# Performance work log

Hardware: AMD Instinct MI355X
Metric: run time of the kernel (lower is better)

Reference implementation:

```python
import jax, jax.numpy as jnp
import numpy as np

N, E = 20000, 320000
IN, HID, OUT, H = 128, 32, 1, 4
EPS = 1e-16  # PyG softmax epsilon


def _p(key, shape, scale=0.05):
    return jax.random.normal(key, shape, dtype=jnp.float32) * scale


def setup_inputs() -> dict:
    key = jax.random.key(0)
    ks = jax.random.split(key, 20)
    d = {
        "x": jax.random.normal(ks[0], (N, IN), dtype=jnp.float32),
        "edge_src": jax.random.randint(ks[1], (E,), 0, N, dtype=jnp.int32),
        "edge_dst": jax.random.randint(ks[2], (E,), 0, N, dtype=jnp.int32),
        # layer 1: TransformerConv(IN, HID, H)  ->  [N, H*HID]
        "W1q": _p(ks[3], (IN, H * HID)), "b1q": jnp.zeros((H * HID,), jnp.float32),
        "W1k": _p(ks[4], (IN, H * HID)), "b1k": jnp.zeros((H * HID,), jnp.float32),
        "W1v": _p(ks[5], (IN, H * HID)), "b1v": jnp.zeros((H * HID,), jnp.float32),
        "W1s": _p(ks[6], (IN, H * HID)), "b1s": jnp.zeros((H * HID,), jnp.float32),
        # layer 2: TransformerConv(H*HID, OUT, H) -> [N, H*OUT]
        "W2q": _p(ks[7], (H * HID, H * OUT)), "b2q": jnp.zeros((H * OUT,), jnp.float32),
        "W2k": _p(ks[8], (H * HID, H * OUT)), "b2k": jnp.zeros((H * OUT,), jnp.float32),
        "W2v": _p(ks[9], (H * HID, H * OUT)), "b2v": jnp.zeros((H * OUT,), jnp.float32),
        "W2s": _p(ks[10], (H * HID, H * OUT)), "b2s": jnp.zeros((H * OUT,), jnp.float32),
        # final nn.Linear(heads, 1)
        "Wl": _p(ks[11], (H, 1)), "bl": jnp.zeros((1,), jnp.float32),
    }
    return d


def transformer_conv(x, src, dst, Wq, bq, Wk, bk, Wv, bv, Ws, bs, heads, ch):
    n = x.shape[0]
    q = (x @ Wq + bq).reshape(n, heads, ch)
    k = (x @ Wk + bk).reshape(n, heads, ch)
    v = (x @ Wv + bv).reshape(n, heads, ch)
    qi, kj, vj = q[dst], k[src], v[src]            # [E,H,C] gathers
    score = (qi * kj).sum(-1) / jnp.sqrt(jnp.float32(ch))  # [E,H]
    m = jax.ops.segment_max(score, dst, num_segments=n)    # segment softmax by target
    e = jnp.exp(score - m[dst])
    s = jax.ops.segment_sum(e, dst, num_segments=n)
    alpha = e / (s[dst] + EPS)                              # [E,H]
    agg = jax.ops.segment_sum(alpha[:, :, None] * vj, dst, num_segments=n)  # [N,H,C]
    return agg.reshape(n, heads * ch) + x @ Ws + bs          # concat + root skip


def reference(x, edge_src, edge_dst,
              W1q, b1q, W1k, b1k, W1v, b1v, W1s, b1s,
              W2q, b2q, W2k, b2k, W2v, b2v, W2s, b2s,
              Wl, bl):
    h = transformer_conv(x, edge_src, edge_dst, W1q, b1q, W1k, b1k, W1v, b1v, W1s, b1s, H, HID)
    h = jax.nn.relu(h)  # dropout is identity in eval
    h = transformer_conv(h, edge_src, edge_dst, W2q, b2q, W2k, b2k, W2v, b2v, W2s, b2s, H, OUT)
    y = h @ Wl + bl                      # [N,1]
    return y.mean(axis=0, keepdims=True)  # [1,1]
```

## Files before the change

### kernel.cpp

```cpp
#include <hip/hip_runtime.h>
#include <math.h>

static constexpr float EPS_PYG = 1e-16f;
static constexpr float INV_SQRT32 = 0.17677669529663687f;

__global__ void deg_kernel(const int* __restrict__ dst, int* __restrict__ deg, int E) {
    int e = blockIdx.x * blockDim.x + threadIdx.x;
    if (e < E) atomicAdd(&deg[dst[e]], 1);
}

__global__ __launch_bounds__(1024) void scan_kernel(const int* __restrict__ deg,
                                                    int* __restrict__ row_off, int n) {
    const int t = threadIdx.x;
    const int CH = (n + 1023) >> 10;
    const int base = t * CH;
    int vals[32];
    int sum = 0;
#pragma unroll 4
    for (int i = 0; i < CH; ++i) {
        int idx = base + i;
        int v = (idx < n) ? deg[idx] : 0;
        sum += v;
        vals[i] = sum;
    }
    const int lane = t & 63;
    const int wid = t >> 6;
    int wsum = sum;
#pragma unroll
    for (int off = 1; off < 64; off <<= 1) {
        int o = __shfl_up(wsum, off, 64);
        if (lane >= off) wsum += o;
    }
    __shared__ int wtot[16];
    if (lane == 63) wtot[wid] = wsum;
    __syncthreads();
    if (t < 64) {
        int v = (t < 16) ? wtot[t] : 0;
        int inc = v;
#pragma unroll
        for (int off = 1; off < 16; off <<= 1) {
            int o = __shfl_up(inc, off, 64);
            if (t >= off) inc += o;
        }
        if (t < 16) wtot[t] = inc - v;
    }
    __syncthreads();
    const int toff = wtot[wid] + (wsum - sum);
    if (t == 0) row_off[0] = 0;
#pragma unroll 4
    for (int i = 0; i < CH; ++i) {
        int idx = base + i;
        if (idx < n) row_off[idx + 1] = toff + vals[i];
    }
}

__global__ void scatter_kernel(const int* __restrict__ src, const int* __restrict__ dst,
                               const int* __restrict__ row_off, int* __restrict__ cursor,
                               int* __restrict__ csr_src, int E) {
    int e = blockIdx.x * blockDim.x + threadIdx.x;
    if (e < E) {
        int d = dst[e];
        int pos = row_off[d] + atomicAdd(&cursor[d], 1);
        csr_src[pos] = src[e];
    }
}

__global__ __launch_bounds__(256) void gemm1_kernel(
    const float* __restrict__ X,
    const float* __restrict__ Wq, const float* __restrict__ Wk,
    const float* __restrict__ Wv, const float* __restrict__ Wsk,
    const float* __restrict__ bq, const float* __restrict__ bk,
    const float* __restrict__ bv, const float* __restrict__ bsk,
    float* __restrict__ Q, float* __restrict__ KV, float* __restrict__ S, int n)
{
    __shared__ float Xs[64][68];
    __shared__ float Wt[64][64];

    const int mat    = blockIdx.y >> 1;
    const int colblk = blockIdx.y & 1;
    const float* W    = (mat == 0) ? Wq : (mat == 1) ? Wk : (mat == 2) ? Wv : Wsk;
    const float* bias = (mat == 0) ? bq : (mat == 1) ? bk : (mat == 2) ? bv : bsk;
    float*       C    = (mat == 0) ? Q  : (mat == 3) ? S  : KV;
    const int strideF4 = (mat == 1 || mat == 2) ? 64 : 32;
    const int baseF4   = (mat == 2) ? 32 : 0;

    const int r0  = blockIdx.x * 64;
    const int tid = threadIdx.x;
    const int i0 = (tid >> 4) * 4;
    const int j0 = (tid & 15) * 4;
    float acc[4][4] = {};

#pragma unroll
    for (int kb = 0; kb < 2; ++kb) {
        for (int f = tid; f < 1024; f += 256) {
            int row = f >> 4, c4 = f & 15;
            float4 val = make_float4(0.f, 0.f, 0.f, 0.f);
            if (r0 + row < n)
                val = ((const float4*)X)[(size_t)(r0 + row) * 32 + kb * 16 + c4];
            *(float4*)&Xs[row][c4 * 4] = val;
        }
        for (int f = tid; f < 1024; f += 256) {
            int row = f >> 4, c4 = f & 15;
            float4 val = ((const float4*)W)[(kb * 64 + row) * 32 + colblk * 16 + c4];
            *(float4*)&Wt[row][c4 * 4] = val;
        }
        __syncthreads();

#pragma unroll 4
        for (int k = 0; k < 64; ++k) {
            float a0 = Xs[i0 + 0][k];
            float a1 = Xs[i0 + 1][k];
            float a2 = Xs[i0 + 2][k];
            float a3 = Xs[i0 + 3][k];
            float4 b = *(const float4*)&Wt[k][j0];
            acc[0][0] += a0 * b.x; acc[0][1] += a0 * b.y; acc[0][2] += a0 * b.z; acc[0][3] += a0 * b.w;
            acc[1][0] += a1 * b.x; acc[1][1] += a1 * b.y; acc[1][2] += a1 * b.z; acc[1][3] += a1 * b.w;
            acc[2][0] += a2 * b.x; acc[2][1] += a2 * b.y; acc[2][2] += a2 * b.z; acc[2][3] += a2 * b.w;
            acc[3][0] += a3 * b.x; acc[3][1] += a3 * b.y; acc[3][2] += a3 * b.z; acc[3][3] += a3 * b.w;
        }
        __syncthreads();
    }

    const int jg = colblk * 64 + j0;
    float4 b4 = *(const float4*)&bias[jg];
#pragma unroll
    for (int r = 0; r < 4; ++r) {
        int row = r0 + i0 + r;
        if (row < n) {
            float4 o = make_float4(acc[r][0] + b4.x, acc[r][1] + b4.y,
                                   acc[r][2] + b4.z, acc[r][3] + b4.w);
            ((float4*)C)[(size_t)row * strideF4 + baseF4 + (jg >> 2)] = o;
        }
    }
}

__global__ __launch_bounds__(128) void l1_agg_kernel(
    const float* __restrict__ Q, const float* __restrict__ KV,
    const float* __restrict__ S,
    const int* __restrict__ row_off, const int* __restrict__ csr_src,
    float* __restrict__ H1, int n)
{
    const int node = blockIdx.x;
    const int t = threadIdx.x;
    const float q = Q[(size_t)node * 128 + t];
    const int beg = row_off[node], end = row_off[node + 1];

    float l = 0.f, acc = 0.f;
    int pos = beg;
    for (; pos + 4 <= end; pos += 4) {
        int s0 = csr_src[pos];
        int s1 = csr_src[pos + 1];
        int s2 = csr_src[pos + 2];
        int s3 = csr_src[pos + 3];
        const float* b0 = KV + (size_t)s0 * 256;
        const float* b1 = KV + (size_t)s1 * 256;
        const float* b2 = KV + (size_t)s2 * 256;
        const float* b3 = KV + (size_t)s3 * 256;
        float k0 = b0[t], k1 = b1[t], k2 = b2[t], k3 = b3[t];
        float v0 = b0[128 + t], v1 = b1[128 + t], v2 = b2[128 + t], v3 = b3[128 + t];
        float p0 = q * k0, p1 = q * k1, p2 = q * k2, p3 = q * k3;
        p0 += __shfl_xor(p0, 16, 32); p1 += __shfl_xor(p1, 16, 32);
        p2 += __shfl_xor(p2, 16, 32); p3 += __shfl_xor(p3, 16, 32);
        p0 += __shfl_xor(p0, 8, 32);  p1 += __shfl_xor(p1, 8, 32);
        p2 += __shfl_xor(p2, 8, 32);  p3 += __shfl_xor(p3, 8, 32);
        p0 += __shfl_xor(p0, 4, 32);  p1 += __shfl_xor(p1, 4, 32);
        p2 += __shfl_xor(p2, 4, 32);  p3 += __shfl_xor(p3, 4, 32);
        p0 += __shfl_xor(p0, 2, 32);  p1 += __shfl_xor(p1, 2, 32);
        p2 += __shfl_xor(p2, 2, 32);  p3 += __shfl_xor(p3, 2, 32);
        p0 += __shfl_xor(p0, 1, 32);  p1 += __shfl_xor(p1, 1, 32);
        p2 += __shfl_xor(p2, 1, 32);  p3 += __shfl_xor(p3, 1, 32);
        float e0 = __expf(p0 * INV_SQRT32);
        float e1 = __expf(p1 * INV_SQRT32);
        float e2 = __expf(p2 * INV_SQRT32);
        float e3 = __expf(p3 * INV_SQRT32);
        l   += (e0 + e1) + (e2 + e3);
        acc += (e0 * v0 + e1 * v1) + (e2 * v2 + e3 * v3);
    }
    for (; pos < end; ++pos) {
        int s0 = csr_src[pos];
        const float* b0 = KV + (size_t)s0 * 256;
        float k0 = b0[t], v0 = b0[128 + t];
        float p0 = q * k0;
        p0 += __shfl_xor(p0, 16, 32);
        p0 += __shfl_xor(p0, 8, 32);
        p0 += __shfl_xor(p0, 4, 32);
        p0 += __shfl_xor(p0, 2, 32);
        p0 += __shfl_xor(p0, 1, 32);
        float e0 = __expf(p0 * INV_SQRT32);
        l += e0;
        acc += e0 * v0;
    }
    float out = acc / (l + EPS_PYG) + S[(size_t)node * 128 + t];
    H1[(size_t)node * 128 + t] = fmaxf(out, 0.f);
}

__global__ __launch_bounds__(256) void gemm2_kernel(
    const float* __restrict__ H1,
    const float* __restrict__ Wq, const float* __restrict__ Wk,
    const float* __restrict__ Wv, const float* __restrict__ Wsk,
    const float* __restrict__ bq, const float* __restrict__ bk,
    const float* __restrict__ bv, const float* __restrict__ bsk,
    float4* __restrict__ Q2, float4* __restrict__ K2,
    float4* __restrict__ V2, float4* __restrict__ S2, int n)
{
    __shared__ float Hs[64][129];
    __shared__ float Wt[128][16];
    __shared__ float bt[16];

    const int tid = threadIdx.x;
    const int r0 = blockIdx.x * 64;

    for (int i = tid; i < 2048; i += 256) {
        int row = i >> 4, col = i & 15;
        int mt = col >> 2, c = col & 3;
        const float* Wm = (mt == 0) ? Wq : (mt == 1) ? Wk : (mt == 2) ? Wv : Wsk;
        Wt[row][col] = Wm[row * 4 + c];
    }
    if (tid < 16) {
        int mt = tid >> 2;
        const float* bm = (mt == 0) ? bq : (mt == 1) ? bk : (mt == 2) ? bv : bsk;
        bt[tid] = bm[tid & 3];
    }
    for (int f = tid; f < 2048; f += 256) {
        int row = f >> 5, c4 = f & 31;
        float4 val = make_float4(0.f, 0.f, 0.f, 0.f);
        if (r0 + row < n) val = ((const float4*)H1)[(size_t)(r0 + row) * 32 + c4];
        Hs[row][c4 * 4 + 0] = val.x;
        Hs[row][c4 * 4 + 1] = val.y;
        Hs[row][c4 * 4 + 2] = val.z;
        Hs[row][c4 * 4 + 3] = val.w;
    }
    __syncthreads();

    const int nl = tid & 63;
    const int jg = tid >> 6;
    float a0 = 0.f, a1 = 0.f, a2 = 0.f, a3 = 0.f;
#pragma unroll 4
    for (int k = 0; k < 128; ++k) {
        float h = Hs[nl][k];
        a0 += h * Wt[k][jg * 4 + 0];
        a1 += h * Wt[k][jg * 4 + 1];
        a2 += h * Wt[k][jg * 4 + 2];
        a3 += h * Wt[k][jg * 4 + 3];
    }
    int node = r0 + nl;
    if (node < n) {
        float4 o = make_float4(a0 + bt[jg * 4 + 0], a1 + bt[jg * 4 + 1],
                               a2 + bt[jg * 4 + 2], a3 + bt[jg * 4 + 3]);
        float4* Cm = (jg == 0) ? Q2 : (jg == 1) ? K2 : (jg == 2) ? V2 : S2;
        Cm[node] = o;
    }
}

__global__ void init_out_kernel(float* __restrict__ out, const float* __restrict__ bl) {
    out[0] = bl[0];
}

__global__ __launch_bounds__(256) void l2_agg_kernel(
    const float4* __restrict__ Q2, const float4* __restrict__ K2,
    const float4* __restrict__ V2, const float4* __restrict__ S2,
    const int* __restrict__ row_off, const int* __restrict__ csr_src,
    const float* __restrict__ Wl, float* __restrict__ out, int n, float invn)
{
    const int nd = blockIdx.x * 256 + threadIdx.x;
    float y = 0.f;
    if (nd < n) {
        float4 q = Q2[nd];
        float l0 = 0.f, l1 = 0.f, l2 = 0.f, l3 = 0.f;
        float a0 = 0.f, a1 = 0.f, a2 = 0.f, a3 = 0.f;
        const int beg = row_off[nd], end = row_off[nd + 1];
        for (int pos = beg; pos < end; ++pos) {
            int src = csr_src[pos];
            float4 k = K2[src];
            float4 v = V2[src];
            float e0 = __expf(q.x * k.x);
            float e1 = __expf(q.y * k.y);
            float e2 = __expf(q.z * k.z);
            float e3 = __expf(q.w * k.w);
            l0 += e0; a0 += e0 * v.x;
            l1 += e1; a1 += e1 * v.y;
            l2 += e2; a2 += e2 * v.z;
            l3 += e3; a3 += e3 * v.w;
        }
        float4 sk = S2[nd];
        float h0 = a0 / (l0 + EPS_PYG) + sk.x;
        float h1 = a1 / (l1 + EPS_PYG) + sk.y;
        float h2 = a2 / (l2 + EPS_PYG) + sk.z;
        float h3 = a3 / (l3 + EPS_PYG) + sk.w;
        y = (h0 * Wl[0] + h1 * Wl[1] + h2 * Wl[2] + h3 * Wl[3]) * invn;
    }
    __shared__ float red[256];
    red[threadIdx.x] = y;
    __syncthreads();
    for (int off = 128; off > 0; off >>= 1) {
        if (threadIdx.x < (unsigned)off) red[threadIdx.x] += red[threadIdx.x + off];
        __syncthreads();
    }
    if (threadIdx.x == 0) atomicAdd(out, red[0]);
}

extern "C" void kernel_launch(void* const* d_in, const int* in_sizes, int n_in,
                              void* d_out, int out_size, void* d_ws, size_t ws_size,
                              hipStream_t stream) {
    const float* x        = (const float*)d_in[0];
    const int*   edge_src = (const int*)d_in[1];
    const int*   edge_dst = (const int*)d_in[2];
    const float* W1q = (const float*)d_in[3];  const float* b1q = (const float*)d_in[4];
    const float* W1k = (const float*)d_in[5];  const float* b1k = (const float*)d_in[6];
    const float* W1v = (const float*)d_in[7];  const float* b1v = (const float*)d_in[8];
    const float* W1s = (const float*)d_in[9];  const float* b1s = (const float*)d_in[10];
    const float* W2q = (const float*)d_in[11]; const float* b2q = (const float*)d_in[12];
    const float* W2k = (const float*)d_in[13]; const float* b2k = (const float*)d_in[14];
    const float* W2v = (const float*)d_in[15]; const float* b2v = (const float*)d_in[16];
    const float* W2s = (const float*)d_in[17]; const float* b2s = (const float*)d_in[18];
    const float* Wl  = (const float*)d_in[19]; const float* bl  = (const float*)d_in[20];

    const int N = in_sizes[0] / 128;
    const int E = in_sizes[1];
    float* out = (float*)d_out;

    float* ws  = (float*)d_ws;
    size_t off = 0;
    float* Q1 = ws + off; off += (size_t)N * 128;
    float* KV = ws + off; off += (size_t)N * 256;
    float* S1 = ws + off; off += (size_t)N * 128;
    float* H1 = ws + off; off += (size_t)N * 128;
    float* q2 = ws + off; off += (size_t)N * 4;
    float* k2 = ws + off; off += (size_t)N * 4;
    float* v2 = ws + off; off += (size_t)N * 4;
    float* s2 = ws + off; off += (size_t)N * 4;
    int* ibase   = (int*)(ws + off);
    int* deg     = ibase;
    int* cursor  = ibase + N;
    int* row_off = ibase + 2 * N;
    int* csr_src = ibase + 3 * N + 1;

    hipMemsetAsync(deg, 0, (size_t)2 * N * sizeof(int), stream);
    deg_kernel<<<(E + 255) / 256, 256, 0, stream>>>(edge_dst, deg, E);
    scan_kernel<<<1, 1024, 0, stream>>>(deg, row_off, N);
    scatter_kernel<<<(E + 255) / 256, 256, 0, stream>>>(edge_src, edge_dst, row_off,
                                                        cursor, csr_src, E);

    {
        dim3 grid((N + 63) / 64, 8);
        gemm1_kernel<<<grid, 256, 0, stream>>>(x, W1q, W1k, W1v, W1s,
                                               b1q, b1k, b1v, b1s,
                                               Q1, KV, S1, N);
    }
    l1_agg_kernel<<<N, 128, 0, stream>>>(Q1, KV, S1, row_off, csr_src, H1, N);

    gemm2_kernel<<<(N + 63) / 64, 256, 0, stream>>>(H1, W2q, W2k, W2v, W2s,
                                                    b2q, b2k, b2v, b2s,
                                                    (float4*)q2, (float4*)k2,
                                                    (float4*)v2, (float4*)s2, N);
    init_out_kernel<<<1, 1, 0, stream>>>(out, bl);
    l2_agg_kernel<<<(N + 255) / 256, 256, 0, stream>>>((const float4*)q2, (const float4*)k2,
                                                       (const float4*)v2, (const float4*)s2,
                                                       row_off, csr_src, Wl, out, N,
                                                       1.0f / (float)N);
}
```

Baseline: 257.7 us.

## Use bf16 MFMA for layer-1 projections and pack K/V as bf16 pairs

```diff
diff --git a/kernel.cpp b/kernel.cpp
--- a/kernel.cpp
+++ b/kernel.cpp
@@ -3,6 +3,21 @@
 
 static constexpr float EPS_PYG = 1e-16f;
 static constexpr float INV_SQRT32 = 0.17677669529663687f;
+
+typedef short bf16x8 __attribute__((ext_vector_type(8)));
+typedef float f32x4 __attribute__((ext_vector_type(4)));
+
+__device__ inline unsigned short f2bf(float f) {
+    union { float f; unsigned u; } x; x.f = f;
+    unsigned r = x.u + 0x7FFFu + ((x.u >> 16) & 1u);
+    return (unsigned short)(r >> 16);
+}
+__device__ inline float bf_hi(unsigned u) {
+    union { unsigned u; float f; } x; x.u = u & 0xFFFF0000u; return x.f;
+}
+__device__ inline float bf_lo(unsigned u) {
+    union { unsigned u; float f; } x; x.u = u << 16; return x.f;
+}
 
 __global__ void deg_kernel(const int* __restrict__ dst, int* __restrict__ deg, int E) {
     int e = blockIdx.x * blockDim.x + threadIdx.x;
@@ -65,77 +80,82 @@
     }
 }
 
-__global__ __launch_bounds__(256) void gemm1_kernel(
-    const float* __restrict__ X,
+__global__ __launch_bounds__(256) void prep_kernel(
+    const float4* __restrict__ X, ushort4* __restrict__ Xb, int total4,
     const float* __restrict__ Wq, const float* __restrict__ Wk,
     const float* __restrict__ Wv, const float* __restrict__ Wsk,
+    unsigned short* __restrict__ Wbt)
+{
+    const int b = blockIdx.x;
+    if (b < 4) {
+        const float* W = (b == 0) ? Wq : (b == 1) ? Wk : (b == 2) ? Wv : Wsk;
+        for (int i = threadIdx.x; i < 16384; i += 256) {
+            int k = i >> 7, nn = i & 127;
+            Wbt[b * 16384 + nn * 128 + k] = f2bf(W[i]);
+        }
+    } else {
+        int i = (b - 4) * 256 + threadIdx.x;
+        if (i < total4) {
+            float4 v = X[i];
+            ushort4 o;
+            o.x = f2bf(v.x); o.y = f2bf(v.y); o.z = f2bf(v.z); o.w = f2bf(v.w);
+            Xb[i] = o;
+        }
+    }
+}
+
+__global__ __launch_bounds__(256) void gemm1_mfma(
+    const unsigned short* __restrict__ Xb, const unsigned short* __restrict__ Wbt,
     const float* __restrict__ bq, const float* __restrict__ bk,
     const float* __restrict__ bv, const float* __restrict__ bsk,
-    float* __restrict__ Q, float* __restrict__ KV, float* __restrict__ S, int n)
-{
-    __shared__ float Xs[64][68];
-    __shared__ float Wt[64][64];
-
-    const int mat    = blockIdx.y >> 1;
-    const int colblk = blockIdx.y & 1;
-    const float* W    = (mat == 0) ? Wq : (mat == 1) ? Wk : (mat == 2) ? Wv : Wsk;
+    float* __restrict__ Q, unsigned int* __restrict__ KV,
+    float* __restrict__ S, int n)
+{
+    const int mat = blockIdx.y;
+    const unsigned short* W = Wbt + (size_t)mat * 16384;
     const float* bias = (mat == 0) ? bq : (mat == 1) ? bk : (mat == 2) ? bv : bsk;
-    float*       C    = (mat == 0) ? Q  : (mat == 3) ? S  : KV;
-    const int strideF4 = (mat == 1 || mat == 2) ? 64 : 32;
-    const int baseF4   = (mat == 2) ? 32 : 0;
-
-    const int r0  = blockIdx.x * 64;
-    const int tid = threadIdx.x;
-    const int i0 = (tid >> 4) * 4;
-    const int j0 = (tid & 15) * 4;
-    float acc[4][4] = {};
-
-#pragma unroll
-    for (int kb = 0; kb < 2; ++kb) {
-        for (int f = tid; f < 1024; f += 256) {
-            int row = f >> 4, c4 = f & 15;
-            float4 val = make_float4(0.f, 0.f, 0.f, 0.f);
-            if (r0 + row < n)
-                val = ((const float4*)X)[(size_t)(r0 + row) * 32 + kb * 16 + c4];
-            *(float4*)&Xs[row][c4 * 4] = val;
-        }
-        for (int f = tid; f < 1024; f += 256) {
-            int row = f >> 4, c4 = f & 15;
-            float4 val = ((const float4*)W)[(kb * 64 + row) * 32 + colblk * 16 + c4];
-            *(float4*)&Wt[row][c4 * 4] = val;
-        }
-        __syncthreads();
-
-#pragma unroll 4
-        for (int k = 0; k < 64; ++k) {
-            float a0 = Xs[i0 + 0][k];
-            float a1 = Xs[i0 + 1][k];
-            float a2 = Xs[i0 + 2][k];
-            float a3 = Xs[i0 + 3][k];
-            float4 b = *(const float4*)&Wt[k][j0];
-            acc[0][0] += a0 * b.x; acc[0][1] += a0 * b.y; acc[0][2] += a0 * b.z; acc[0][3] += a0 * b.w;
-            acc[1][0] += a1 * b.x; acc[1][1] += a1 * b.y; acc[1][2] += a1 * b.z; acc[1][3] += a1 * b.w;
-            acc[2][0] += a2 * b.x; acc[2][1] += a2 * b.y; acc[2][2] += a2 * b.z; acc[2][3] += a2 * b.w;
-            acc[3][0] += a3 * b.x; acc[3][1] += a3 * b.y; acc[3][2] += a3 * b.z; acc[3][3] += a3 * b.w;
-        }
-        __syncthreads();
-    }
-
-    const int jg = colblk * 64 + j0;
-    float4 b4 = *(const float4*)&bias[jg];
-#pragma unroll
-    for (int r = 0; r < 4; ++r) {
-        int row = r0 + i0 + r;
-        if (row < n) {
-            float4 o = make_float4(acc[r][0] + b4.x, acc[r][1] + b4.y,
-                                   acc[r][2] + b4.z, acc[r][3] + b4.w);
-            ((float4*)C)[(size_t)row * strideF4 + baseF4 + (jg >> 2)] = o;
+
+    const int tid  = threadIdx.x;
+    const int wave = tid >> 6;
+    const int lane = tid & 63;
+    const int m    = lane & 15;
+    const int quad = lane >> 4;
+    const int r0   = blockIdx.x * 64 + wave * 16;
+
+    int arow = r0 + m;
+    if (arow >= n) arow = n - 1;
+
+    f32x4 acc[8] = {};
+#pragma unroll
+    for (int kc = 0; kc < 128; kc += 32) {
+        bf16x8 a = *(const bf16x8*)(Xb + (size_t)arow * 128 + kc + quad * 8);
+#pragma unroll
+        for (int ct = 0; ct < 8; ++ct) {
+            bf16x8 bfr = *(const bf16x8*)(W + (ct * 16 + m) * 128 + kc + quad * 8);
+            acc[ct] = __builtin_amdgcn_mfma_f32_16x16x32_bf16(a, bfr, acc[ct], 0, 0, 0);
+        }
+    }
+
+#pragma unroll
+    for (int ct = 0; ct < 8; ++ct) {
+        const int col = ct * 16 + m;
+        const float bb = bias[col];
+#pragma unroll
+        for (int r = 0; r < 4; ++r) {
+            const int row = r0 + quad * 4 + r;
+            if (row < n) {
+                float val = acc[ct][r] + bb;
+                size_t idx = (size_t)row * 128 + col;
+                if (mat == 0)      Q[idx] = val;
+                else if (mat == 3) S[idx] = val;
+                else ((unsigned short*)KV)[idx * 2 + ((mat == 1) ? 1 : 0)] = f2bf(val);
+            }
         }
     }
 }
 
 __global__ __launch_bounds__(128) void l1_agg_kernel(
-    const float* __restrict__ Q, const float* __restrict__ KV,
+    const float* __restrict__ Q, const unsigned int* __restrict__ KV,
     const float* __restrict__ S,
     const int* __restrict__ row_off, const int* __restrict__ csr_src,
     float* __restrict__ H1, int n)
@@ -152,13 +172,12 @@
         int s1 = csr_src[pos + 1];
         int s2 = csr_src[pos + 2];
         int s3 = csr_src[pos + 3];
-        const float* b0 = KV + (size_t)s0 * 256;
-        const float* b1 = KV + (size_t)s1 * 256;
-        const float* b2 = KV + (size_t)s2 * 256;
-        const float* b3 = KV + (size_t)s3 * 256;
-        float k0 = b0[t], k1 = b1[t], k2 = b2[t], k3 = b3[t];
-        float v0 = b0[128 + t], v1 = b1[128 + t], v2 = b2[128 + t], v3 = b3[128 + t];
-        float p0 = q * k0, p1 = q * k1, p2 = q * k2, p3 = q * k3;
+        unsigned u0 = KV[(size_t)s0 * 128 + t];
+        unsigned u1 = KV[(size_t)s1 * 128 + t];
+        unsigned u2 = KV[(size_t)s2 * 128 + t];
+        unsigned u3 = KV[(size_t)s3 * 128 + t];
+        float p0 = q * bf_hi(u0), p1 = q * bf_hi(u1);
+        float p2 = q * bf_hi(u2), p3 = q * bf_hi(u3);
         p0 += __shfl_xor(p0, 16, 32); p1 += __shfl_xor(p1, 16, 32);
         p2 += __shfl_xor(p2, 16, 32); p3 += __shfl_xor(p3, 16, 32);
         p0 += __shfl_xor(p0, 8, 32);  p1 += __shfl_xor(p1, 8, 32);
@@ -174,13 +193,12 @@
         float e2 = __expf(p2 * INV_SQRT32);
         float e3 = __expf(p3 * INV_SQRT32);
         l   += (e0 + e1) + (e2 + e3);
-        acc += (e0 * v0 + e1 * v1) + (e2 * v2 + e3 * v3);
+        acc += (e0 * bf_lo(u0) + e1 * bf_lo(u1)) + (e2 * bf_lo(u2) + e3 * bf_lo(u3));
     }
     for (; pos < end; ++pos) {
         int s0 = csr_src[pos];
-        const float* b0 = KV + (size_t)s0 * 256;
-        float k0 = b0[t], v0 = b0[128 + t];
-        float p0 = q * k0;
+        unsigned u0 = KV[(size_t)s0 * 128 + t];
+        float p0 = q * bf_hi(u0);
         p0 += __shfl_xor(p0, 16, 32);
         p0 += __shfl_xor(p0, 8, 32);
         p0 += __shfl_xor(p0, 4, 32);
@@ -188,7 +206,7 @@
         p0 += __shfl_xor(p0, 1, 32);
         float e0 = __expf(p0 * INV_SQRT32);
         l += e0;
-        acc += e0 * v0;
+        acc += e0 * bf_lo(u0);
     }
     float out = acc / (l + EPS_PYG) + S[(size_t)node * 128 + t];
     H1[(size_t)node * 128 + t] = fmaxf(out, 0.f);
@@ -321,14 +339,16 @@
 
     float* ws  = (float*)d_ws;
     size_t off = 0;
-    float* Q1 = ws + off; off += (size_t)N * 128;
-    float* KV = ws + off; off += (size_t)N * 256;
-    float* S1 = ws + off; off += (size_t)N * 128;
-    float* H1 = ws + off; off += (size_t)N * 128;
-    float* q2 = ws + off; off += (size_t)N * 4;
-    float* k2 = ws + off; off += (size_t)N * 4;
-    float* v2 = ws + off; off += (size_t)N * 4;
-    float* s2 = ws + off; off += (size_t)N * 4;
+    float*        Q1  = ws + off; off += (size_t)N * 128;
+    unsigned int* KV  = (unsigned int*)(ws + off); off += (size_t)N * 128;
+    float*        S1  = ws + off; off += (size_t)N * 128;
+    float*        H1  = ws + off; off += (size_t)N * 128;
+    float*        q2  = ws + off; off += (size_t)N * 4;
+    float*        k2  = ws + off; off += (size_t)N * 4;
+    float*        v2  = ws + off; off += (size_t)N * 4;
+    float*        s2  = ws + off; off += (size_t)N * 4;
+    unsigned short* Xb  = (unsigned short*)(ws + off); off += (size_t)N * 64;
+    unsigned short* Wbt = (unsigned short*)(ws + off); off += 4 * 16384 / 2;
     int* ibase   = (int*)(ws + off);
     int* deg     = ibase;
     int* cursor  = ibase + N;
@@ -341,11 +361,14 @@
     scatter_kernel<<<(E + 255) / 256, 256, 0, stream>>>(edge_src, edge_dst, row_off,
                                                         cursor, csr_src, E);
 
+    const int total4 = N * 32;
+    prep_kernel<<<4 + (total4 + 255) / 256, 256, 0, stream>>>(
+        (const float4*)x, (ushort4*)Xb, total4, W1q, W1k, W1v, W1s, Wbt);
+
     {
-        dim3 grid((N + 63) / 64, 8);
-        gemm1_kernel<<<grid, 256, 0, stream>>>(x, W1q, W1k, W1v, W1s,
-                                               b1q, b1k, b1v, b1s,
-                                               Q1, KV, S1, N);
+        dim3 grid((N + 63) / 64, 4);
+        gemm1_mfma<<<grid, 256, 0, stream>>>(Xb, Wbt, b1q, b1k, b1v, b1s,
+                                             Q1, KV, S1, N);
     }
     l1_agg_kernel<<<N, 128, 0, stream>>>(Q1, KV, S1, row_off, csr_src, H1, N);
 
```

After: 258.1 us. No clear change (+0.1%).
